# Kernel optimization log

Hardware: AMD Instinct MI355X
Metric: run time of the kernel (lower is better)

## Reference

```python
import jax, jax.numpy as jnp
import numpy as np

N_NODES = 100000
N_EDGES = 1600000
N_GRAPHS = 128
IN_F, H_F, OUT_F, HID, NCLS = 128, 128, 64, 10, 10

def setup_inputs() -> dict:
    key = jax.random.key(0)
    ks = jax.random.split(key, 12)
    feats = jax.random.normal(ks[0], (N_NODES, IN_F), dtype=jnp.float32)
    src = jax.random.randint(ks[1], (N_EDGES,), 0, N_NODES, dtype=jnp.int32)
    dst = jax.random.randint(ks[2], (N_EDGES,), 0, N_NODES, dtype=jnp.int32)
    graph_ids = jnp.sort(jax.random.randint(ks[3], (N_NODES,), 0, N_GRAPHS, dtype=jnp.int32))
    def glorot(k, shape):
        fan = shape[0] + shape[1]
        return jax.random.normal(k, shape, dtype=jnp.float32) * jnp.sqrt(2.0 / fan)
    return {
        'feats': feats, 'src': src, 'dst': dst, 'graph_ids': graph_ids,
        'W1': glorot(ks[4], (IN_F, H_F)), 'b1': jnp.zeros((H_F,), jnp.float32),
        'W2': glorot(ks[5], (H_F, OUT_F)), 'b2': jnp.zeros((OUT_F,), jnp.float32),
        'fcW1': glorot(ks[6], (OUT_F, HID)), 'fcb1': jnp.zeros((HID,), jnp.float32),
        'fcW2': glorot(ks[7], (HID, NCLS)), 'fcb2': jnp.zeros((NCLS,), jnp.float32),
    }

def _graph_conv(x, W, b, src, dst):
    # DGL GraphConv, norm='both': D_dst^{-1/2} A D_src^{-1/2} X W + b
    ones = jnp.ones((src.shape[0],), x.dtype)
    deg_out = jnp.clip(jax.ops.segment_sum(ones, src, num_segments=N_NODES), 1.0)
    deg_in = jnp.clip(jax.ops.segment_sum(ones, dst, num_segments=N_NODES), 1.0)
    x = x * jax.lax.rsqrt(deg_out)[:, None]
    m = jax.ops.segment_sum(x[src], dst, num_segments=N_NODES)  # gather-scatter over edges
    m = m * jax.lax.rsqrt(deg_in)[:, None]
    return m @ W + b

def reference(feats, src, dst, graph_ids, W1, b1, W2, b2, fcW1, fcb1, fcW2, fcb2):
    h = jax.nn.relu(_graph_conv(feats, W1, b1, src, dst))
    h = jax.nn.relu(_graph_conv(h, W2, b2, src, dst))
    # dgl.mean_nodes: per-graph mean pooling
    sums = jax.ops.segment_sum(h, graph_ids, num_segments=N_GRAPHS)
    counts = jnp.clip(jax.ops.segment_sum(jnp.ones((N_NODES,), h.dtype), graph_ids, num_segments=N_GRAPHS), 1.0)
    pooled = sums / counts[:, None]  # [G, OUT_F]
    z = jax.nn.relu(pooled @ fcW1 + fcb1)
    return jax.nn.softmax(z @ fcW2 + fcb2, axis=1)
```

## Files before the change

### kernel.cpp

```cpp
#include <hip/hip_runtime.h>
#include <hip/hip_bf16.h>

#define N_NODES 100000
#define N_EDGES 1600000
#define N_GRAPHS 128
#define IN_F 128
#define H_F 128
#define OUT_F 64
#define HID 10
#define NCLS 10
#define XPAD 136
#define BSH 7
#define NBUCK 782
#define SBLK 128
#define EPB (N_EDGES / SBLK)
#define NB_PREP 4

typedef __attribute__((ext_vector_type(8))) short bf16x8;
typedef __attribute__((ext_vector_type(4))) float f32x4;
typedef __attribute__((ext_vector_type(2))) float f32x2;

__device__ __forceinline__ float bl(unsigned int u) { return __uint_as_float(u << 16); }
__device__ __forceinline__ float bh(unsigned int u) { return __uint_as_float(u & 0xffff0000u); }

__global__ __launch_bounds__(1024) void k_hist2(const int* __restrict__ src, const int* __restrict__ dst,
                                                int* __restrict__ Pd, int* __restrict__ Ps,
                                                const float* __restrict__ W1, const float* __restrict__ W2,
                                                unsigned short* __restrict__ Wt1, unsigned short* __restrict__ Wt2,
                                                float* __restrict__ part) {
    __shared__ int hd[NBUCK];
    __shared__ int hs[NBUCK];
    const int blk = blockIdx.x;
    if (blk < SBLK) {
        for (int i = threadIdx.x; i < NBUCK; i += 1024) { hd[i] = 0; hs[i] = 0; }
        __syncthreads();
        const int base = blk * EPB;
        for (int i = threadIdx.x; i < EPB; i += 1024) {
            atomicAdd(&hd[dst[base + i] >> BSH], 1);
            atomicAdd(&hs[src[base + i] >> BSH], 1);
        }
        __syncthreads();
        for (int b = threadIdx.x; b < NBUCK; b += 1024) {
            Pd[b * SBLK + blk] = hd[b];
            Ps[b * SBLK + blk] = hs[b];
        }
    } else {
        int t = (blk - SBLK) * 1024 + threadIdx.x;
        const int stride = NB_PREP * 1024;
        for (int i = t; i < 128 * 128; i += stride) {
            int c = i >> 7, k = i & 127;
            __hip_bfloat16 v = __float2bfloat16(W1[k * 128 + c]);
            Wt1[i] = *(unsigned short*)&v;
        }
        for (int i = t; i < 64 * 128; i += stride) {
            int c = i >> 7, k = i & 127;
            __hip_bfloat16 v = __float2bfloat16(W2[k * 64 + c]);
            Wt2[i] = *(unsigned short*)&v;
        }
        for (int i = t; i < N_GRAPHS * 64; i += stride) part[i] = 0.f;
    }
}

__global__ __launch_bounds__(SBLK) void k_scanA(int* __restrict__ Pd, int* __restrict__ Ps,
                                                int* __restrict__ Td, int* __restrict__ Ts) {
    __shared__ int sc[SBLK];
    const int b = blockIdx.x;
    const int t = threadIdx.x;
    int* P = (b < NBUCK) ? Pd : Ps;
    int* T = (b < NBUCK) ? Td : Ts;
    const int bb = (b < NBUCK) ? b : b - NBUCK;
    int v = P[bb * SBLK + t];
    sc[t] = v;
    __syncthreads();
    for (int off = 1; off < SBLK; off <<= 1) {
        int u = (t >= off) ? sc[t - off] : 0;
        __syncthreads();
        sc[t] += u;
        __syncthreads();
    }
    P[bb * SBLK + t] = sc[t] - v;
    if (t == SBLK - 1) T[bb] = sc[SBLK - 1];
}

__global__ __launch_bounds__(1024) void k_scanB(const int* __restrict__ Td, const int* __restrict__ Ts,
                                                int* __restrict__ Bd, int* __restrict__ Bs) {
    __shared__ int sc[1024];
    const int t = threadIdx.x;
    int v = (t < NBUCK) ? Td[t] : 0;
    sc[t] = v;
    __syncthreads();
    for (int off = 1; off < 1024; off <<= 1) {
        int u = (t >= off) ? sc[t - off] : 0;
        __syncthreads();
        sc[t] += u;
        __syncthreads();
    }
    if (t < NBUCK) Bd[t] = sc[t] - v;
    if (t == NBUCK - 1) Bd[NBUCK] = sc[t];
    __syncthreads();
    int v2 = (t < NBUCK) ? Ts[t] : 0;
    sc[t] = v2;
    __syncthreads();
    for (int off = 1; off < 1024; off <<= 1) {
        int u = (t >= off) ? sc[t - off] : 0;
        __syncthreads();
        sc[t] += u;
        __syncthreads();
    }
    if (t < NBUCK) Bs[t] = sc[t] - v2;
    if (t == NBUCK - 1) Bs[NBUCK] = sc[t];
}

__global__ __launch_bounds__(1024) void k_scatter(const int* __restrict__ src, const int* __restrict__ dst,
                                                  const int* __restrict__ Pd, const int* __restrict__ Ps,
                                                  const int* __restrict__ Bd, const int* __restrict__ Bs,
                                                  unsigned int* __restrict__ pb, unsigned char* __restrict__ sb) {
    __shared__ int tk[NBUCK];
    const int b = blockIdx.x;
    const bool isPb = b < SBLK;
    const int blk = isPb ? b : b - SBLK;
    if (isPb) {
        for (int i = threadIdx.x; i < NBUCK; i += 1024) tk[i] = Bd[i] + Pd[i * SBLK + blk];
    } else {
        for (int i = threadIdx.x; i < NBUCK; i += 1024) tk[i] = Bs[i] + Ps[i * SBLK + blk];
    }
    __syncthreads();
    const int base = blk * EPB;
    if (isPb) {
        for (int i = threadIdx.x; i < EPB; i += 1024) {
            int d = dst[base + i];
            int s = src[base + i];
            int bd = d >> BSH;
            int pos = atomicAdd(&tk[bd], 1);
            pb[pos] = ((unsigned)s << 7) | (unsigned)(d & 127);
        }
    } else {
        for (int i = threadIdx.x; i < EPB; i += 1024) {
            int s = src[base + i];
            int bs = s >> BSH;
            int pos = atomicAdd(&tk[bs], 1);
            sb[pos] = (unsigned char)(s & 127);
        }
    }
}

__global__ __launch_bounds__(256) void k_finalize(const unsigned int* __restrict__ pb, const int* __restrict__ Bd,
                                                  const unsigned char* __restrict__ sb, const int* __restrict__ Bs,
                                                  int* __restrict__ rp, int* __restrict__ cnt_out,
                                                  int* __restrict__ cols) {
    __shared__ int cnt[128];
    __shared__ int exc[128];
    __shared__ int tick[128];
    __shared__ int h[128];
    __shared__ int sc[128];
    const int b = blockIdx.x;
    const int tid = threadIdx.x;
    if (tid < 128) { cnt[tid] = 0; tick[tid] = 0; h[tid] = 0; }
    __syncthreads();
    const int e0 = Bd[b], e1 = Bd[b + 1];
    for (int i = e0 + tid; i < e1; i += 256) atomicAdd(&cnt[pb[i] & 127], 1);
    const int f0 = Bs[b], f1 = Bs[b + 1];
    for (int i = f0 + tid; i < f1; i += 256) atomicAdd(&h[sb[i]], 1);
    __syncthreads();
    if (tid < 128) sc[tid] = cnt[tid];
    __syncthreads();
    for (int off = 1; off < 128; off <<= 1) {
        int u = (tid < 128 && tid >= off) ? sc[tid - off] : 0;
        __syncthreads();
        if (tid < 128) sc[tid] += u;
        __syncthreads();
    }
    if (tid < 128) exc[tid] = sc[tid] - cnt[tid];
    __syncthreads();
    const int node0 = b << BSH;
    if (tid < 128 && node0 + tid < N_NODES) {
        rp[node0 + tid] = e0 + exc[tid];
        cnt_out[node0 + tid] = h[tid];
    }
    if (b == NBUCK - 1 && tid == 0) rp[N_NODES] = N_EDGES;
    for (int i = e0 + tid; i < e1; i += 256) {
        unsigned int p = pb[i];
        int loc = p & 127;
        int t = atomicAdd(&tick[loc], 1);
        cols[e0 + exc[loc] + t] = (int)(p >> 7);
    }
}

__global__ __launch_bounds__(256) void k_gemm1(const float* __restrict__ X,
                                               const unsigned short* __restrict__ Wt,
                                               const int* __restrict__ cnt_out,
                                               unsigned char* __restrict__ Gout) {
    __shared__ __align__(16) unsigned short Xs[32 * XPAD];
    __shared__ __align__(16) unsigned short Ws[128 * XPAD];
    const int tid = threadIdx.x;
    const int row0 = blockIdx.x * 32;

    {
        const float4* X4 = (const float4*)X;
#pragma unroll
        for (int j = 0; j < 4; j++) {
            int i = tid + 256 * j;
            int r = i >> 5, k4 = i & 31;
            float4 x = X4[(size_t)(row0 + r) * 32 + k4];
            __hip_bfloat162 lo = __float22bfloat162_rn({x.x, x.y});
            __hip_bfloat162 hi = __float22bfloat162_rn({x.z, x.w});
            uint2 u;
            u.x = *(unsigned int*)&lo;
            u.y = *(unsigned int*)&hi;
            *(uint2*)&Xs[r * XPAD + k4 * 4] = u;
        }
    }
    {
        const uint2* W2 = (const uint2*)Wt;
#pragma unroll
        for (int j = 0; j < 16; j++) {
            int i = tid + 256 * j;
            int cc = i >> 5, kk = i & 31;
            uint2 u = W2[(size_t)cc * 32 + kk];
            *(uint2*)&Ws[cc * XPAD + kk * 4] = u;
        }
    }
    __syncthreads();

    const int lane = tid & 63;
    const int wv = tid >> 6;
    const int m = lane & 15;
    const int q = lane >> 4;
    const int cg = wv * 32;

    f32x4 acc00 = {0.f, 0.f, 0.f, 0.f}, acc01 = {0.f, 0.f, 0.f, 0.f};
    f32x4 acc10 = {0.f, 0.f, 0.f, 0.f}, acc11 = {0.f, 0.f, 0.f, 0.f};
#pragma unroll
    for (int ks = 0; ks < 4; ks++) {
        int kb = ks * 32 + q * 8;
        bf16x8 a0 = *(const bf16x8*)&Xs[m * XPAD + kb];
        bf16x8 a1 = *(const bf16x8*)&Xs[(16 + m) * XPAD + kb];
        bf16x8 b0 = *(const bf16x8*)&Ws[(cg + m) * XPAD + kb];
        bf16x8 b1 = *(const bf16x8*)&Ws[(cg + 16 + m) * XPAD + kb];
        acc00 = __builtin_amdgcn_mfma_f32_16x16x32_bf16(a0, b0, acc00, 0, 0, 0);
        acc01 = __builtin_amdgcn_mfma_f32_16x16x32_bf16(a0, b1, acc01, 0, 0, 0);
        acc10 = __builtin_amdgcn_mfma_f32_16x16x32_bf16(a1, b0, acc10, 0, 0, 0);
        acc11 = __builtin_amdgcn_mfma_f32_16x16x32_bf16(a1, b1, acc11, 0, 0, 0);
    }
#pragma unroll
    for (int r = 0; r < 4; r++) {
        int rowA = row0 + q * 4 + r;
        int rowB = rowA + 16;
        float sA = rsqrtf((float)max(cnt_out[rowA], 1));
        float sB = rsqrtf((float)max(cnt_out[rowB], 1));
        unsigned int pkA = __builtin_amdgcn_cvt_pk_fp8_f32(acc00[r] * sA, acc01[r] * sA, 0, false);
        unsigned int pkB = __builtin_amdgcn_cvt_pk_fp8_f32(acc10[r] * sB, acc11[r] * sB, 0, false);
        unsigned char* gA = Gout + (size_t)rowA * 128 + cg + m;
        gA[0]  = (unsigned char)(pkA & 0xffu);
        gA[16] = (unsigned char)((pkA >> 8) & 0xffu);
        unsigned char* gB = Gout + (size_t)rowB * 128 + cg + m;
        gB[0]  = (unsigned char)(pkB & 0xffu);
        gB[16] = (unsigned char)((pkB >> 8) & 0xffu);
    }
}

template <int TOTF, bool XBF16, bool OUT_FP8>
__global__ __launch_bounds__(256) void k_gemm_mfma(const void* __restrict__ Xv,
                                                   const unsigned short* __restrict__ Wt,
                                                   const int* __restrict__ cnt_out,
                                                   void* __restrict__ GoutV) {
    __shared__ __align__(16) unsigned short Xs[32 * XPAD];
    __shared__ __align__(16) unsigned short Ws[64 * XPAD];
    const int tid = threadIdx.x;
    const int cbase = blockIdx.y * 64;
    const int row0 = blockIdx.x * 32;

    if constexpr (XBF16) {
        const uint2* X2 = (const uint2*)Xv;
#pragma unroll
        for (int j = 0; j < 4; j++) {
            int i = tid + 256 * j;
            int r = i >> 5, kk = i & 31;
            uint2 u = X2[(size_t)(row0 + r) * 32 + kk];
            *(uint2*)&Xs[r * XPAD + kk * 4] = u;
        }
    } else {
        const float4* X4 = (const float4*)Xv;
#pragma unroll
        for (int j = 0; j < 4; j++) {
            int i = tid + 256 * j;
            int r = i >> 5, k4 = i & 31;
            float4 x = X4[(size_t)(row0 + r) * 32 + k4];
            __hip_bfloat162 lo = __float22bfloat162_rn({x.x, x.y});
            __hip_bfloat162 hi = __float22bfloat162_rn({x.z, x.w});
            uint2 u;
            u.x = *(unsigned int*)&lo;
            u.y = *(unsigned int*)&hi;
            *(uint2*)&Xs[r * XPAD + k4 * 4] = u;
        }
    }
    {
        const uint2* W2 = (const uint2*)Wt;
#pragma unroll
        for (int j = 0; j < 8; j++) {
            int i = tid + 256 * j;
            int c = i >> 5, kk = i & 31;
            uint2 u = W2[(size_t)(cbase + c) * 32 + kk];
            *(uint2*)&Ws[c * XPAD + kk * 4] = u;
        }
    }
    __syncthreads();

    const int lane = tid & 63;
    const int wv = tid >> 6;
    const int m = lane & 15;
    const int q = lane >> 4;
    const int roff = (wv & 1) * 16;
    const int coff = (wv >> 1) * 32;

    f32x4 acc0 = {0.f, 0.f, 0.f, 0.f}, acc1 = {0.f, 0.f, 0.f, 0.f};
#pragma unroll
    for (int ks = 0; ks < 4; ks++) {
        int kb = ks * 32 + q * 8;
        bf16x8 a  = *(const bf16x8*)&Xs[(roff + m) * XPAD + kb];
        bf16x8 b0 = *(const bf16x8*)&Ws[(coff + m) * XPAD + kb];
        bf16x8 b1 = *(const bf16x8*)&Ws[(coff + 16 + m) * XPAD + kb];
        acc0 = __builtin_amdgcn_mfma_f32_16x16x32_bf16(a, b0, acc0, 0, 0, 0);
        acc1 = __builtin_amdgcn_mfma_f32_16x16x32_bf16(a, b1, acc1, 0, 0, 0);
    }
#pragma unroll
    for (int r = 0; r < 4; r++) {
        int row = row0 + roff + q * 4 + r;
        float s = rsqrtf((float)max(cnt_out[row], 1));
        int col0 = cbase + coff + m;
        if constexpr (OUT_FP8) {
            unsigned int pk = __builtin_amdgcn_cvt_pk_fp8_f32(acc0[r] * s, acc1[r] * s, 0, false);
            unsigned char* gp = (unsigned char*)GoutV + (size_t)row * TOTF + col0;
            gp[0]  = (unsigned char)(pk & 0xffu);
            gp[16] = (unsigned char)((pk >> 8) & 0xffu);
        } else {
            unsigned short* Gout = (unsigned short*)GoutV;
            __hip_bfloat16 o0 = __float2bfloat16(acc0[r] * s);
            __hip_bfloat16 o1 = __float2bfloat16(acc1[r] * s);
            Gout[(size_t)row * TOTF + col0]      = *(unsigned short*)&o0;
            Gout[(size_t)row * TOTF + col0 + 16] = *(unsigned short*)&o1;
        }
    }
}

__device__ __forceinline__ void tail128(const unsigned short* __restrict__ gl, const int* __restrict__ cols,
                                        int b, int d, int j, f32x2& acc) {
    while (j + 16 <= d) {
        unsigned int u[16];
#pragma unroll
        for (int k = 0; k < 16; k++) { int s = cols[b + j + k]; u[k] = gl[(size_t)s * 64]; }
#pragma unroll
        for (int k = 0; k < 16; k++) acc += __builtin_amdgcn_cvt_pk_f32_fp8(u[k], false);
        j += 16;
    }
    if (j + 8 <= d) {
        unsigned int u[8];
#pragma unroll
        for (int k = 0; k < 8; k++) { int s = cols[b + j + k]; u[k] = gl[(size_t)s * 64]; }
#pragma unroll
        for (int k = 0; k < 8; k++) acc += __builtin_amdgcn_cvt_pk_f32_fp8(u[k], false);
        j += 8;
    }
    if (j + 4 <= d) {
        unsigned int u[4];
#pragma unroll
        for (int k = 0; k < 4; k++) { int s = cols[b + j + k]; u[k] = gl[(size_t)s * 64]; }
#pragma unroll
        for (int k = 0; k < 4; k++) acc += __builtin_amdgcn_cvt_pk_f32_fp8(u[k], false);
        j += 4;
    }
    if (j + 2 <= d) {
        unsigned int u0, u1;
        { int s = cols[b + j];     u0 = gl[(size_t)s * 64]; }
        { int s = cols[b + j + 1]; u1 = gl[(size_t)s * 64]; }
        acc += __builtin_amdgcn_cvt_pk_f32_fp8(u0, false);
        acc += __builtin_amdgcn_cvt_pk_f32_fp8(u1, false);
        j += 2;
    }
    if (j < d) {
        int s = cols[b + j];
        unsigned int u = gl[(size_t)s * 64];
        acc += __builtin_amdgcn_cvt_pk_f32_fp8(u, false);
    }
}

__device__ __forceinline__ void tail64(const unsigned char* __restrict__ gl, const int* __restrict__ cols,
                                       int b, int d, int j, f32x2& acc) {
    while (j + 16 <= d) {
        unsigned int u[16];
#pragma unroll
        for (int k = 0; k < 16; k++) { int s = cols[b + j + k]; u[k] = gl[(size_t)s * 64]; }
#pragma unroll
        for (int k = 0; k < 16; k++) acc += __builtin_amdgcn_cvt_pk_f32_fp8(u[k], false);
        j += 16;
    }
    if (j + 8 <= d) {
        unsigned int u[8];
#pragma unroll
        for (int k = 0; k < 8; k++) { int s = cols[b + j + k]; u[k] = gl[(size_t)s * 64]; }
#pragma unroll
        for (int k = 0; k < 8; k++) acc += __builtin_amdgcn_cvt_pk_f32_fp8(u[k], false);
        j += 8;
    }
    if (j + 4 <= d) {
        unsigned int u[4];
#pragma unroll
        for (int k = 0; k < 4; k++) { int s = cols[b + j + k]; u[k] = gl[(size_t)s * 64]; }
#pragma unroll
        for (int k = 0; k < 4; k++) acc += __builtin_amdgcn_cvt_pk_f32_fp8(u[k], false);
        j += 4;
    }
    if (j + 2 <= d) {
        unsigned int u0, u1;
        { int s = cols[b + j];     u0 = gl[(size_t)s * 64]; }
        { int s = cols[b + j + 1]; u1 = gl[(size_t)s * 64]; }
        acc += __builtin_amdgcn_cvt_pk_f32_fp8(u0, false);
        acc += __builtin_amdgcn_cvt_pk_f32_fp8(u1, false);
        j += 2;
    }
    if (j < d) {
        int s = cols[b + j];
        unsigned int u = gl[(size_t)s * 64];
        acc += __builtin_amdgcn_cvt_pk_f32_fp8(u, false);
    }
}

__global__ __launch_bounds__(256) void k_spmm128f8(const unsigned short* __restrict__ G,
                                                   const int* __restrict__ rp,
                                                   const int* __restrict__ cols,
                                                   const float* __restrict__ bias,
                                                   unsigned int* __restrict__ H) {
    const int lane = threadIdx.x & 63;
    const int wave = threadIdx.x >> 6;
    const int v0 = (blockIdx.x * 4 + wave) * 2;
    const int b0 = __builtin_amdgcn_readfirstlane(rp[v0]);
    const int b1 = __builtin_amdgcn_readfirstlane(rp[v0 + 1]);
    const int e1 = __builtin_amdgcn_readfirstlane(rp[v0 + 2]);
    const int dA = b1 - b0, dB = e1 - b1;
    const unsigned short* gl = G + lane;
    f32x2 aA = {0.f, 0.f}, aB = {0.f, 0.f};
    int ja = 0, jb = 0;
    while (ja + 8 <= dA && jb + 8 <= dB) {
        unsigned int u[8], w[8];
#pragma unroll
        for (int k = 0; k < 8; k++) { int s = cols[b0 + ja + k]; u[k] = gl[(size_t)s * 64]; }
#pragma unroll
        for (int k = 0; k < 8; k++) { int s = cols[b1 + jb + k]; w[k] = gl[(size_t)s * 64]; }
#pragma unroll
        for (int k = 0; k < 8; k++) aA += __builtin_amdgcn_cvt_pk_f32_fp8(u[k], false);
#pragma unroll
        for (int k = 0; k < 8; k++) aB += __builtin_amdgcn_cvt_pk_f32_fp8(w[k], false);
        ja += 8; jb += 8;
    }
    tail128(gl, cols, b0, dA, ja, aA);
    tail128(gl, cols, b1, dB, jb, aB);

    {
        const float rs = rsqrtf((float)max(dA, 1));
        const float2 bb = *(const float2*)&bias[2 * lane];
        __hip_bfloat162 p = __float22bfloat162_rn({fmaxf(fmaf(aA.x, rs, bb.x), 0.f),
                                                   fmaxf(fmaf(aA.y, rs, bb.y), 0.f)});
        H[(size_t)v0 * 64 + lane] = *(unsigned int*)&p;
    }
    {
        const float rs = rsqrtf((float)max(dB, 1));
        const float2 bb = *(const float2*)&bias[2 * lane];
        __hip_bfloat162 p = __float22bfloat162_rn({fmaxf(fmaf(aB.x, rs, bb.x), 0.f),
                                                   fmaxf(fmaf(aB.y, rs, bb.y), 0.f)});
        H[(size_t)(v0 + 1) * 64 + lane] = *(unsigned int*)&p;
    }
}

__global__ __launch_bounds__(256) void k_spmm64f8(const unsigned char* __restrict__ G,
                                                  const int* __restrict__ rp,
                                                  const int* __restrict__ cols,
                                                  const float* __restrict__ bias,
                                                  const int* __restrict__ gid,
                                                  float* __restrict__ part) {
    __shared__ float acc[8][64];
    __shared__ int gv[8];
    const int lane = threadIdx.x & 63;
    const int wave = threadIdx.x >> 6;
    const int vb = blockIdx.x * 8;
    const int v0 = vb + wave * 2;
    const int b0 = __builtin_amdgcn_readfirstlane(rp[v0]);
    const int b1 = __builtin_amdgcn_readfirstlane(rp[v0 + 1]);
    const int e1 = __builtin_amdgcn_readfirstlane(rp[v0 + 2]);
    const int dA = b1 - b0, dB = e1 - b1;
    const unsigned char* gl = G + lane;
    if (threadIdx.x < 8) gv[threadIdx.x] = gid[vb + threadIdx.x];
    f32x2 aA = {0.f, 0.f}, aB = {0.f, 0.f};
    int ja = 0, jb = 0;
    while (ja + 8 <= dA && jb + 8 <= dB) {
        unsigned int u[8], w[8];
#pragma unroll
        for (int k = 0; k < 8; k++) { int s = cols[b0 + ja + k]; u[k] = gl[(size_t)s * 64]; }
#pragma unroll
        for (int k = 0; k < 8; k++) { int s = cols[b1 + jb + k]; w[k] = gl[(size_t)s * 64]; }
#pragma unroll
        for (int k = 0; k < 8; k++) aA += __builtin_amdgcn_cvt_pk_f32_fp8(u[k], false);
#pragma unroll
        for (int k = 0; k < 8; k++) aB += __builtin_amdgcn_cvt_pk_f32_fp8(w[k], false);
        ja += 8; jb += 8;
    }
    tail64(gl, cols, b0, dA, ja, aA);
    tail64(gl, cols, b1, dB, jb, aB);

    const float bbias = bias[lane];
    {
        const float rs = rsqrtf((float)max(dA, 1));
        acc[wave * 2][lane] = fmaxf(fmaf(aA.x, rs, bbias), 0.f);
    }
    {
        const float rs = rsqrtf((float)max(dB, 1));
        acc[wave * 2 + 1][lane] = fmaxf(fmaf(aB.x, rs, bbias), 0.f);
    }
    __syncthreads();
    if (threadIdx.x < 64) {
        const int col = threadIdx.x;
        float sum = acc[0][col];
        int g = gv[0];
#pragma unroll
        for (int r = 1; r < 8; r++) {
            int gr = gv[r];
            float v = acc[r][col];
            if (gr != g) {
                atomicAdd(&part[g * 64 + col], sum);
                sum = v;
                g = gr;
            } else {
                sum += v;
            }
        }
        atomicAdd(&part[g * 64 + col], sum);
    }
}

__global__ __launch_bounds__(64) void k_mlp(const float* __restrict__ part,
                                            const int* __restrict__ gid,
                                            const float* __restrict__ fcW1,
                                            const float* __restrict__ fcb1,
                                            const float* __restrict__ fcW2,
                                            const float* __restrict__ fcb2,
                                            float* __restrict__ out) {
    __shared__ int se[2];
    __shared__ float p[64];
    __shared__ float z[10];
    __shared__ float l[10];
    __shared__ float red[2];
    const int g = blockIdx.x;
    const int t = threadIdx.x;
    if (t < 2) {
        int target = g + t;
        int lo = 0, hi = N_NODES;
        while (lo < hi) {
            int mid = (lo + hi) >> 1;
            if (gid[mid] < target) lo = mid + 1; else hi = mid;
        }
        se[t] = lo;
    }
    __syncthreads();
    const int cnt = max(se[1] - se[0], 1);
    p[t] = part[g * 64 + t] / (float)cnt;
    __syncthreads();
    if (t < 10) {
        float acc = fcb1[t];
        for (int k = 0; k < 64; k++) acc = fmaf(p[k], fcW1[k * 10 + t], acc);
        z[t] = fmaxf(acc, 0.f);
    }
    __syncthreads();
    if (t < 10) {
        float acc = fcb2[t];
        for (int k = 0; k < 10; k++) acc = fmaf(z[k], fcW2[k * 10 + t], acc);
        l[t] = acc;
    }
    __syncthreads();
    if (t == 0) {
        float m = l[0];
        for (int i = 1; i < 10; i++) m = fmaxf(m, l[i]);
        float ssum = 0.f;
        for (int i = 0; i < 10; i++) ssum += expf(l[i] - m);
        red[0] = m;
        red[1] = ssum;
    }
    __syncthreads();
    if (t < 10) out[g * 10 + t] = expf(l[t] - red[0]) / red[1];
}

extern "C" void kernel_launch(void* const* d_in, const int* in_sizes, int n_in,
                              void* d_out, int out_size, void* d_ws, size_t ws_size,
                              hipStream_t stream) {
    const float* feats = (const float*)d_in[0];
    const int* src = (const int*)d_in[1];
    const int* dst = (const int*)d_in[2];
    const int* gid = (const int*)d_in[3];
    const float* W1 = (const float*)d_in[4];
    const float* b1 = (const float*)d_in[5];
    const float* W2 = (const float*)d_in[6];
    const float* b2 = (const float*)d_in[7];
    const float* fcW1 = (const float*)d_in[8];
    const float* fcb1 = (const float*)d_in[9];
    const float* fcW2 = (const float*)d_in[10];
    const float* fcb2 = (const float*)d_in[11];
    float* out = (float*)d_out;

    char* w = (char*)d_ws;
    size_t off = 0;
    auto alloc = [&](size_t bytes) -> void* {
        void* p = w + off;
        off = (off + bytes + 255) & ~(size_t)255;
        return p;
    };
    int* cnt_out = (int*)alloc(N_NODES * 4);
    int* rp      = (int*)alloc((N_NODES + 1) * 4);
    int* cols    = (int*)alloc((size_t)N_EDGES * 4);
    int* Pd      = (int*)alloc(NBUCK * SBLK * 4);
    int* Ps      = (int*)alloc(NBUCK * SBLK * 4);
    int* Td      = (int*)alloc(NBUCK * 4);
    int* Ts      = (int*)alloc(NBUCK * 4);
    int* Bd      = (int*)alloc((NBUCK + 1) * 4);
    int* Bs      = (int*)alloc((NBUCK + 1) * 4);
    unsigned int* pb  = (unsigned int*)alloc((size_t)N_EDGES * 4);
    unsigned char* sb = (unsigned char*)alloc((size_t)N_EDGES);
    unsigned short* Wt1 = (unsigned short*)alloc(128 * 128 * 2);
    unsigned short* Wt2 = (unsigned short*)alloc(64 * 128 * 2);
    unsigned char* g1 = (unsigned char*)alloc((size_t)N_NODES * 128);
    unsigned short* h1 = (unsigned short*)alloc((size_t)N_NODES * 128 * 2);
    unsigned char* g2 = (unsigned char*)alloc((size_t)N_NODES * 64);
    float* part = (float*)alloc((size_t)N_GRAPHS * 64 * 4);

    k_hist2<<<SBLK + NB_PREP, 1024, 0, stream>>>(src, dst, Pd, Ps, W1, W2, Wt1, Wt2, part);
    k_scanA<<<2 * NBUCK, SBLK, 0, stream>>>(Pd, Ps, Td, Ts);
    k_scanB<<<1, 1024, 0, stream>>>(Td, Ts, Bd, Bs);
    k_scatter<<<2 * SBLK, 1024, 0, stream>>>(src, dst, Pd, Ps, Bd, Bs, pb, sb);
    k_finalize<<<NBUCK, 256, 0, stream>>>(pb, Bd, sb, Bs, rp, cnt_out, cols);

    k_gemm1<<<N_NODES / 32, 256, 0, stream>>>(feats, Wt1, cnt_out, g1);
    k_spmm128f8<<<N_NODES / 8, 256, 0, stream>>>((const unsigned short*)g1, rp, cols, b1, (unsigned int*)h1);

    k_gemm_mfma<64, true, true><<<dim3(N_NODES / 32, 1), 256, 0, stream>>>(h1, Wt2, cnt_out, g2);
    k_spmm64f8<<<N_NODES / 8, 256, 0, stream>>>(g2, rp, cols, b2, gid, part);

    k_mlp<<<N_GRAPHS, 64, 0, stream>>>(part, gid, fcW1, fcb1, fcW2, fcb2, out);
}
```

Measured before the change: 258.7 us.

## Fuse second-layer GEMM into first SpMM epilogue via LDS MFMA

The layer-1 SpMM now writes its bf16 ReLU output rows into shared memory and multiplies them by W2 with MFMA inside the same block, emitting fp8 g2 directly. This removes the global h1 buffer write/read and the separate GEMM launch. In exchange each block reloads W2 into LDS, pads 8 rows to a 16-row MFMA tile, and adds a block barrier plus more LDS, which may reduce occupancy for the gather-heavy loop.

```diff
diff --git a/kernel.cpp b/kernel.cpp
--- a/kernel.cpp
+++ b/kernel.cpp
@@ -259,90 +259,6 @@
     }
 }
 
-template <int TOTF, bool XBF16, bool OUT_FP8>
-__global__ __launch_bounds__(256) void k_gemm_mfma(const void* __restrict__ Xv,
-                                                   const unsigned short* __restrict__ Wt,
-                                                   const int* __restrict__ cnt_out,
-                                                   void* __restrict__ GoutV) {
-    __shared__ __align__(16) unsigned short Xs[32 * XPAD];
-    __shared__ __align__(16) unsigned short Ws[64 * XPAD];
-    const int tid = threadIdx.x;
-    const int cbase = blockIdx.y * 64;
-    const int row0 = blockIdx.x * 32;
-
-    if constexpr (XBF16) {
-        const uint2* X2 = (const uint2*)Xv;
-#pragma unroll
-        for (int j = 0; j < 4; j++) {
-            int i = tid + 256 * j;
-            int r = i >> 5, kk = i & 31;
-            uint2 u = X2[(size_t)(row0 + r) * 32 + kk];
-            *(uint2*)&Xs[r * XPAD + kk * 4] = u;
-        }
-    } else {
-        const float4* X4 = (const float4*)Xv;
-#pragma unroll
-        for (int j = 0; j < 4; j++) {
-            int i = tid + 256 * j;
-            int r = i >> 5, k4 = i & 31;
-            float4 x = X4[(size_t)(row0 + r) * 32 + k4];
-            __hip_bfloat162 lo = __float22bfloat162_rn({x.x, x.y});
-            __hip_bfloat162 hi = __float22bfloat162_rn({x.z, x.w});
-            uint2 u;
-            u.x = *(unsigned int*)&lo;
-            u.y = *(unsigned int*)&hi;
-            *(uint2*)&Xs[r * XPAD + k4 * 4] = u;
-        }
-    }
-    {
-        const uint2* W2 = (const uint2*)Wt;
-#pragma unroll
-        for (int j = 0; j < 8; j++) {
-            int i = tid + 256 * j;
-            int c = i >> 5, kk = i & 31;
-            uint2 u = W2[(size_t)(cbase + c) * 32 + kk];
-            *(uint2*)&Ws[c * XPAD + kk * 4] = u;
-        }
-    }
-    __syncthreads();
-
-    const int lane = tid & 63;
-    const int wv = tid >> 6;
-    const int m = lane & 15;
-    const int q = lane >> 4;
-    const int roff = (wv & 1) * 16;
-    const int coff = (wv >> 1) * 32;
-
-    f32x4 acc0 = {0.f, 0.f, 0.f, 0.f}, acc1 = {0.f, 0.f, 0.f, 0.f};
-#pragma unroll
-    for (int ks = 0; ks < 4; ks++) {
-        int kb = ks * 32 + q * 8;
-        bf16x8 a  = *(const bf16x8*)&Xs[(roff + m) * XPAD + kb];
-        bf16x8 b0 = *(const bf16x8*)&Ws[(coff + m) * XPAD + kb];
-        bf16x8 b1 = *(const bf16x8*)&Ws[(coff + 16 + m) * XPAD + kb];
-        acc0 = __builtin_amdgcn_mfma_f32_16x16x32_bf16(a, b0, acc0, 0, 0, 0);
-        acc1 = __builtin_amdgcn_mfma_f32_16x16x32_bf16(a, b1, acc1, 0, 0, 0);
-    }
-#pragma unroll
-    for (int r = 0; r < 4; r++) {
-        int row = row0 + roff + q * 4 + r;
-        float s = rsqrtf((float)max(cnt_out[row], 1));
-        int col0 = cbase + coff + m;
-        if constexpr (OUT_FP8) {
-            unsigned int pk = __builtin_amdgcn_cvt_pk_fp8_f32(acc0[r] * s, acc1[r] * s, 0, false);
-            unsigned char* gp = (unsigned char*)GoutV + (size_t)row * TOTF + col0;
-            gp[0]  = (unsigned char)(pk & 0xffu);
-            gp[16] = (unsigned char)((pk >> 8) & 0xffu);
-        } else {
-            unsigned short* Gout = (unsigned short*)GoutV;
-            __hip_bfloat16 o0 = __float2bfloat16(acc0[r] * s);
-            __hip_bfloat16 o1 = __float2bfloat16(acc1[r] * s);
-            Gout[(size_t)row * TOTF + col0]      = *(unsigned short*)&o0;
-            Gout[(size_t)row * TOTF + col0 + 16] = *(unsigned short*)&o1;
-        }
-    }
-}
-
 __device__ __forceinline__ void tail128(const unsigned short* __restrict__ gl, const int* __restrict__ cols,
                                         int b, int d, int j, f32x2& acc) {
     while (j + 16 <= d) {
@@ -429,10 +345,29 @@
                                                    const int* __restrict__ rp,
                                                    const int* __restrict__ cols,
                                                    const float* __restrict__ bias,
-                                                   unsigned int* __restrict__ H) {
-    const int lane = threadIdx.x & 63;
-    const int wave = threadIdx.x >> 6;
-    const int v0 = (blockIdx.x * 4 + wave) * 2;
+                                                   const int* __restrict__ cnt_out,
+                                                   const unsigned short* __restrict__ Wt,
+                                                   unsigned char* __restrict__ G2out) {
+    __shared__ __align__(16) unsigned short hs[16 * XPAD];
+    __shared__ __align__(16) unsigned short Ws[64 * XPAD];
+    const int tid = threadIdx.x;
+    const int lane = tid & 63;
+    const int wave = tid >> 6;
+    const int vb = blockIdx.x * 8;
+    const int v0 = vb + wave * 2;
+
+    {
+        const uint2* W2 = (const uint2*)Wt;
+#pragma unroll
+        for (int j = 0; j < 8; j++) {
+            int i = tid + 256 * j;
+            int c = i >> 5, kk = i & 31;
+            uint2 u = W2[(size_t)c * 32 + kk];
+            *(uint2*)&Ws[c * XPAD + kk * 4] = u;
+        }
+    }
+    for (int i = tid; i < 8 * XPAD; i += 256) hs[8 * XPAD + i] = 0;
+
     const int b0 = __builtin_amdgcn_readfirstlane(rp[v0]);
     const int b1 = __builtin_amdgcn_readfirstlane(rp[v0 + 1]);
     const int e1 = __builtin_amdgcn_readfirstlane(rp[v0 + 2]);
@@ -455,19 +390,42 @@
     tail128(gl, cols, b0, dA, ja, aA);
     tail128(gl, cols, b1, dB, jb, aB);
 
+    const float2 bb = *(const float2*)&bias[2 * lane];
     {
         const float rs = rsqrtf((float)max(dA, 1));
-        const float2 bb = *(const float2*)&bias[2 * lane];
         __hip_bfloat162 p = __float22bfloat162_rn({fmaxf(fmaf(aA.x, rs, bb.x), 0.f),
                                                    fmaxf(fmaf(aA.y, rs, bb.y), 0.f)});
-        H[(size_t)v0 * 64 + lane] = *(unsigned int*)&p;
+        *(unsigned int*)&hs[(wave * 2) * XPAD + 2 * lane] = *(unsigned int*)&p;
     }
     {
         const float rs = rsqrtf((float)max(dB, 1));
-        const float2 bb = *(const float2*)&bias[2 * lane];
         __hip_bfloat162 p = __float22bfloat162_rn({fmaxf(fmaf(aB.x, rs, bb.x), 0.f),
                                                    fmaxf(fmaf(aB.y, rs, bb.y), 0.f)});
-        H[(size_t)(v0 + 1) * 64 + lane] = *(unsigned int*)&p;
+        *(unsigned int*)&hs[(wave * 2 + 1) * XPAD + 2 * lane] = *(unsigned int*)&p;
+    }
+    __syncthreads();
+
+    const int m = lane & 15;
+    const int q = lane >> 4;
+    const int coff = wave * 16;
+    f32x4 acc = {0.f, 0.f, 0.f, 0.f};
+#pragma unroll
+    for (int ks = 0; ks < 4; ks++) {
+        int kb = ks * 32 + q * 8;
+        bf16x8 a = *(const bf16x8*)&hs[m * XPAD + kb];
+        bf16x8 b = *(const bf16x8*)&Ws[(coff + m) * XPAD + kb];
+        acc = __builtin_amdgcn_mfma_f32_16x16x32_bf16(a, b, acc, 0, 0, 0);
+    }
+#pragma unroll
+    for (int r = 0; r < 4; r++) {
+        int row = q * 4 + r;
+        if (row < 8) {
+            int node = vb + row;
+            float s = rsqrtf((float)max(cnt_out[node], 1));
+            float v = acc[r] * s;
+            unsigned int pk = __builtin_amdgcn_cvt_pk_fp8_f32(v, v, 0, false);
+            G2out[(size_t)node * 64 + coff + m] = (unsigned char)(pk & 0xffu);
+        }
     }
 }
 
@@ -625,7 +583,6 @@
     unsigned short* Wt1 = (unsigned short*)alloc(128 * 128 * 2);
     unsigned short* Wt2 = (unsigned short*)alloc(64 * 128 * 2);
     unsigned char* g1 = (unsigned char*)alloc((size_t)N_NODES * 128);
-    unsigned short* h1 = (unsigned short*)alloc((size_t)N_NODES * 128 * 2);
     unsigned char* g2 = (unsigned char*)alloc((size_t)N_NODES * 64);
     float* part = (float*)alloc((size_t)N_GRAPHS * 64 * 4);
 
@@ -636,9 +593,9 @@
     k_finalize<<<NBUCK, 256, 0, stream>>>(pb, Bd, sb, Bs, rp, cnt_out, cols);
 
     k_gemm1<<<N_NODES / 32, 256, 0, stream>>>(feats, Wt1, cnt_out, g1);
-    k_spmm128f8<<<N_NODES / 8, 256, 0, stream>>>((const unsigned short*)g1, rp, cols, b1, (unsigned int*)h1);
-
-    k_gemm_mfma<64, true, true><<<dim3(N_NODES / 32, 1), 256, 0, stream>>>(h1, Wt2, cnt_out, g2);
+
+    k_spmm128f8<<<N_NODES / 8, 256, 0, stream>>>((const unsigned short*)g1, rp, cols, b1, cnt_out, Wt2, g2);
+
     k_spmm64f8<<<N_NODES / 8, 256, 0, stream>>>(g2, rp, cols, b2, gid, part);
 
     k_mlp<<<N_GRAPHS, 64, 0, stream>>>(part, gid, fcW1, fcb1, fcW2, fcb2, out);
```

New measurement: 266.6 us. 1.03x slower.
